# Performance work log

Measured on AMD Instinct MI355X. Metric: run time of the kernel, lower is better.

The kernel has to match this reference:

```python
import jax, jax.numpy as jnp
import numpy as np

N_EDGES = 8_388_608      # total synapses (flat weight vector length)
NUM_TYPES = 200          # number of unique edge types (ragged groups)
STRENGTH = 1e-3          # regularizer strength (cast to float32 as in the TF module)


def setup_inputs() -> dict:
    key = jax.random.key(0)
    k1, k2, k3 = jax.random.split(key, 3)
    # Edges pre-sorted by edge type -> contiguous segments (equivalent to the
    # RaggedTensor.from_value_rowids grouping built in __init__).
    segment_ids = jnp.sort(
        jax.random.randint(k1, (N_EDGES,), 0, NUM_TYPES, dtype=jnp.int32))
    x = jax.random.normal(k2, (N_EDGES,), dtype=jnp.float32)
    init_raw = jax.random.normal(k3, (N_EDGES,), dtype=jnp.float32)
    # __init__ sorts the initial weights within each edge-type group; since
    # segment_ids is already sorted, lexsort with segment_ids as the primary
    # key sorts values within each contiguous segment.
    order = jnp.lexsort((init_raw, segment_ids))
    initial_sorted = init_raw[order]
    return {"x": x, "initial_sorted": initial_sorted, "segment_ids": segment_ids}


def reference(x, initial_sorted, segment_ids):
    x = x.astype(jnp.float32)
    # Segmented sort of the current weights: primary key = edge type,
    # secondary key = value. Equivalent to tf.sort(x_i) per ragged group.
    order = jnp.lexsort((x, segment_ids))
    x_sorted = x[order]                       # [n_edges], sorted within each group
    diff = jnp.abs(x_sorted - initial_sorted)  # per-edge |sorted(x) - sorted(y)|
    sums = jax.ops.segment_sum(diff, segment_ids, num_segments=NUM_TYPES)
    counts = jax.ops.segment_sum(jnp.ones_like(diff), segment_ids,
                                 num_segments=NUM_TYPES)
    emd = sums / jnp.maximum(counts, 1.0)      # per-group Wasserstein-1 (mean L1)
    return jnp.mean(emd) * jnp.float32(STRENGTH)
```

## Files before the change

### kernel.cpp

```cpp
#include <hip/hip_runtime.h>
#include <hip/hip_bf16.h>

#define NSEG 200
#define STRENGTH 1e-3f
#define NFB 16384
#define FSCALE (16384.0f / 12.0f)
#define BT 1024
#define SPLIT 5
#define WINCAP 9728
#define EPT 10
#define PSTRIDE (NFB + 8)
#define PCH 8192
#define SLICE_E 8200

__device__ __forceinline__ int fbin_of(float v) {
    float t = (v + 6.0f) * FSCALE;
    int b = (int)floorf(t);
    return b < 0 ? 0 : (b > NFB - 1 ? NFB - 1 : b);
}

__global__ void __launch_bounds__(BT)
k_hist(const float* __restrict__ x, const int* __restrict__ seg,
       int* __restrict__ seg_starts, float* __restrict__ segSums,
       unsigned* __restrict__ gcur, unsigned short* __restrict__ pfxg,
       int* __restrict__ Bg, int* __restrict__ Bpos, int N) {
    __shared__ unsigned hw[NFB / 2];
    __shared__ unsigned wsum[16];
    __shared__ int sh2[3];
    int s = blockIdx.x;
    int t = threadIdx.x;
    if (t <= 1) {
        int key = s + t;
        int lo = 0, hi = N;
        while (lo < hi) { int mid = (lo + hi) >> 1; if (seg[mid] < key) lo = mid + 1; else hi = mid; }
        sh2[t] = lo;
    }
    if (t < 8) gcur[s * 8 + t] = 0u;
    if (t == 2) segSums[s] = 0.f;
    for (int k = t; k < NFB / 2; k += BT) hw[k] = 0;
    __syncthreads();
    int st = sh2[0], en = sh2[1];
    if (t == 3) { seg_starts[s] = st; if (s == NSEG - 1) seg_starts[NSEG] = N; }
    int n = en - st;
    const float* xs = x + st;
    if (n > 0) {
        int head = min(n, (int)((4 - (st & 3)) & 3));
        for (int k = t; k < head; k += BT) { int f = fbin_of(xs[k]); atomicAdd(&hw[f >> 1], 1u << ((f & 1) * 16)); }
        int nv = (n - head) >> 2;
        const float4* xs4 = (const float4*)(xs + head);
        for (int j = t; j < nv; j += BT) {
            float4 v = xs4[j];
            int f0 = fbin_of(v.x), f1 = fbin_of(v.y), f2 = fbin_of(v.z), f3 = fbin_of(v.w);
            atomicAdd(&hw[f0 >> 1], 1u << ((f0 & 1) * 16));
            atomicAdd(&hw[f1 >> 1], 1u << ((f1 & 1) * 16));
            atomicAdd(&hw[f2 >> 1], 1u << ((f2 & 1) * 16));
            atomicAdd(&hw[f3 >> 1], 1u << ((f3 & 1) * 16));
        }
        for (int k = head + nv * 4 + t; k < n; k += BT) { int f = fbin_of(xs[k]); atomicAdd(&hw[f >> 1], 1u << ((f & 1) * 16)); }
    }
    __syncthreads();
    unsigned wv[8]; unsigned run = 0;
    #pragma unroll
    for (int i = 0; i < 8; ++i) {
        unsigned w = hw[t * 8 + i];
        unsigned c0 = w & 0xffffu, c1 = w >> 16;
        wv[i] = run | ((run + c0) << 16);
        run += c0 + c1;
    }
    unsigned incl = run;
    for (int off = 1; off < 64; off <<= 1) {
        unsigned nv2 = __shfl_up(incl, off, 64);
        if ((t & 63) >= off) incl += nv2;
    }
    if ((t & 63) == 63) wsum[t >> 6] = incl;
    __syncthreads();
    unsigned wb = 0; int myw = t >> 6;
    #pragma unroll
    for (int j = 0; j < 16; ++j) wb += (j < myw) ? wsum[j] : 0u;
    unsigned base = wb + incl - run;
    unsigned bb = base | (base << 16);
    unsigned short* pp = pfxg + (size_t)s * PSTRIDE;
    #pragma unroll
    for (int i = 0; i < 8; ++i) {
        unsigned pw = wv[i] + bb;
        hw[t * 8 + i] = pw;
        ((unsigned*)pp)[t * 8 + i] = pw;
    }
    if (t == BT - 1) { pp[NFB] = (unsigned short)(base + run); sh2[2] = (int)(base + run); }
    __syncthreads();
    int nsh = sh2[2];
    if (t == 0) { Bg[s * 8 + 0] = 0; Bg[s * 8 + SPLIT] = NFB; Bpos[s * 8 + 0] = 0; Bpos[s * 8 + SPLIT] = nsh; }
    if (t >= 1 && t < SPLIT) {
        int target = (int)(((long)t * nsh) / SPLIT);
        int lo = 0, hi = NFB - 1;
        while (lo < hi) {
            int mid = (lo + hi) >> 1;
            int pv = (int)((hw[(mid + 1) >> 1] >> (((mid + 1) & 1) * 16)) & 0xffffu);
            if (pv > target) hi = mid; else lo = mid + 1;
        }
        Bg[s * 8 + t] = lo;
        Bpos[s * 8 + t] = (int)((hw[lo >> 1] >> ((lo & 1) * 16)) & 0xffffu);
    }
}

__global__ void __launch_bounds__(1024)
k_part(const float* __restrict__ x, const int* __restrict__ seg_starts,
       const int* __restrict__ Bg, const int* __restrict__ Bpos,
       unsigned* __restrict__ gcur, float* __restrict__ part, int N) {
    __shared__ int sst[NSEG + 1];
    __shared__ unsigned hh[16][12];
    __shared__ int gb[10];
    __shared__ int sB[8];
    int t = threadIdx.x;
    for (int k = t; k < NSEG + 1; k += 1024) sst[k] = seg_starts[k];
    if (t < 192) ((unsigned*)hh)[t] = 0u;
    __syncthreads();
    int base = blockIdx.x * PCH;
    if (base >= N) return;
    int lo = 0, hi = NSEG - 1;
    while (lo < hi) { int mid = (lo + hi) >> 1; if (base < sst[mid + 1]) hi = mid; else lo = mid + 1; }
    int s0 = lo, bnd = sst[s0 + 1];
    if (t < 4) sB[t] = Bg[s0 * 8 + 1 + t];
    else if (t < 8 && s0 + 1 <= NSEG) sB[t] = Bg[(s0 + 1) * 8 + 1 + (t - 4)];
    __syncthreads();
    int grp = t >> 6;
    float vv[8]; unsigned pk[8];
    const float4* x4 = (const float4*)(x + base);
    #pragma unroll
    for (int it = 0; it < 2; ++it) {
        int j = it * 1024 + t;
        int gi = base + j * 4;
        float4 v4;
        if (gi + 3 < N) v4 = x4[j];
        else v4 = make_float4(0.f, 0.f, 0.f, 0.f);
        #pragma unroll
        for (int e = 0; e < 4; ++e) {
            int i = it * 4 + e;
            float v = (e == 0) ? v4.x : (e == 1) ? v4.y : (e == 2) ? v4.z : v4.w;
            vv[i] = v;
            int g = gi + e;
            if (g < N) {
                int off = (g >= bnd) ? 4 : 0;
                int f = fbin_of(v);
                int p = (f >= sB[off]) + (f >= sB[off + 1]) + (f >= sB[off + 2]) + (f >= sB[off + 3]);
                int sp = (off >> 2) * 5 + p;
                unsigned lr = atomicAdd(&hh[grp][sp], 1u);
                pk[i] = ((unsigned)sp << 10) | lr;
            } else pk[i] = 0xffffffffu;
        }
    }
    __syncthreads();
    if (t < 10) {
        unsigned run = 0;
        #pragma unroll
        for (int g = 0; g < 16; ++g) { unsigned c = hh[g][t]; hh[g][t] = run; run += c; }
        int s = s0 + (t >= 5);
        int p = (t >= 5) ? t - 5 : t;
        int rsv = 0;
        if (run > 0) rsv = (int)atomicAdd(&gcur[s * 8 + p], run);
        gb[t] = sst[s] + Bpos[s * 8 + p] + rsv;
    }
    __syncthreads();
    #pragma unroll
    for (int i = 0; i < 8; ++i) {
        if (pk[i] == 0xffffffffu) continue;
        int sp = (int)(pk[i] >> 10);
        int lr = (int)(pk[i] & 1023u);
        part[gb[sp] + (int)hh[grp][sp] + lr] = vv[i];
    }
}

__global__ void __launch_bounds__(BT)
k_seg(const float* __restrict__ part, const float* __restrict__ y,
      const int* __restrict__ seg_starts, const unsigned short* __restrict__ pfxg,
      const int* __restrict__ Bg, float* __restrict__ segSums) {
    __shared__ unsigned short slice[SLICE_E];
    __shared__ unsigned cur[2056];
    __shared__ __align__(16) float win[WINCAP + 4];
    __shared__ float warr[16];
    int s = blockIdx.x % NSEG;
    int p = blockIdx.x / NSEG;
    int t = threadIdx.x;
    int st = seg_starts[s], en = seg_starts[s + 1];
    int n = en - st;
    if (n <= 0) return;
    const unsigned short* pp = pfxg + (size_t)s * PSTRIDE;
    int Fa = Bg[s * 8 + p], Fb = Bg[s * 8 + p + 1];
    int spanc = Fb - Fa;
    int w0 = pp[Fa], w1 = pp[Fb];
    int wsz = w1 - w0;
    if (wsz <= 0) return;
    const float* ps = part + st + w0;
    bool sliced = (spanc + 1) <= SLICE_E;

    float rv[EPT]; int rr[EPT];
    if (sliced) {
        for (int k = t; k <= spanc; k += BT) slice[k] = pp[Fa + k];
        for (int k = t; k < ((spanc + 4) >> 2); k += BT) cur[k] = 0u;
        __syncthreads();
        int head = min(wsz, (int)((4 - ((st + w0) & 3)) & 3));
        for (int k = t; k < head; k += BT) {
            float v = ps[k];
            int i = fbin_of(v) - Fa;
            unsigned shf = (i & 3) * 8;
            unsigned old = atomicAdd(&cur[i >> 2], 1u << shf);
            win[(int)slice[i] - w0 + (int)((old >> shf) & 0xFFu)] = v;
        }
        int nv = (wsz - head) >> 2;
        const float4* ps4 = (const float4*)(ps + head);
        for (int j = t; j < nv; j += BT) {
            float4 v4 = ps4[j];
            #pragma unroll
            for (int e = 0; e < 4; ++e) {
                float v = (e == 0) ? v4.x : (e == 1) ? v4.y : (e == 2) ? v4.z : v4.w;
                int i = fbin_of(v) - Fa;
                unsigned shf = (i & 3) * 8;
                unsigned old = atomicAdd(&cur[i >> 2], 1u << shf);
                win[(int)slice[i] - w0 + (int)((old >> shf) & 0xFFu)] = v;
            }
        }
        for (int k = head + nv * 4 + t; k < wsz; k += BT) {
            float v = ps[k];
            int i = fbin_of(v) - Fa;
            unsigned shf = (i & 3) * 8;
            unsigned old = atomicAdd(&cur[i >> 2], 1u << shf);
            win[(int)slice[i] - w0 + (int)((old >> shf) & 0xFFu)] = v;
        }
        if (t < 4) win[wsz + t] = __builtin_inff();
        __syncthreads();
        #pragma unroll
        for (int e = 0; e < EPT; ++e) {
            int ql = e * BT + t;
            rr[e] = -1;
            if (ql < wsz) {
                float v = win[ql];
                rv[e] = v;
                int i = fbin_of(v) - Fa;
                int ls = (int)slice[i] - w0, le = (int)slice[i + 1] - w0;
                int a = ls & ~3;
                int cnt = a - ls;
                for (int j = a; j < le; j += 4) {
                    float4 qv = *(const float4*)&win[j];
                    cnt += (qv.x < v) + ((qv.x == v) & (j + 0 < ql));
                    cnt += (qv.y < v) + ((qv.y == v) & (j + 1 < ql));
                    cnt += (qv.z < v) + ((qv.z == v) & (j + 2 < ql));
                    cnt += (qv.w < v) + ((qv.w == v) & (j + 3 < ql));
                }
                rr[e] = ls + cnt;
            }
        }
    } else {
        for (int k = t; k < wsz; k += BT) win[k] = ps[k];
        if (t < 4) win[wsz + t] = __builtin_inff();
        __syncthreads();
        #pragma unroll
        for (int e = 0; e < EPT; ++e) {
            int ql = e * BT + t;
            rr[e] = -1;
            if (ql < wsz) {
                float v = win[ql];
                rv[e] = v;
                int cnt = 0;
                for (int j = 0; j < wsz; j += 4) {
                    float4 qv = *(const float4*)&win[j];
                    cnt += (qv.x < v) + ((qv.x == v) & (j + 0 < ql));
                    cnt += (qv.y < v) + ((qv.y == v) & (j + 1 < ql));
                    cnt += (qv.z < v) + ((qv.z == v) & (j + 2 < ql));
                    cnt += (qv.w < v) + ((qv.w == v) & (j + 3 < ql));
                }
                rr[e] = cnt;
            }
        }
    }
    __syncthreads();
    #pragma unroll
    for (int e = 0; e < EPT; ++e) {
        if (rr[e] >= 0) win[rr[e]] = rv[e];
    }
    __syncthreads();
    float acc = 0.f;
    const float* yw = y + st + w0;
    int head2 = min(wsz, (int)((4 - ((st + w0) & 3)) & 3));
    for (int k = t; k < head2; k += BT) acc += fabsf(win[k] - yw[k]);
    int nv2 = (wsz - head2) >> 2;
    const float4* yw4 = (const float4*)(yw + head2);
    for (int j = t; j < nv2; j += BT) {
        float4 yv = yw4[j];
        int k = head2 + j * 4;
        acc += fabsf(win[k + 0] - yv.x);
        acc += fabsf(win[k + 1] - yv.y);
        acc += fabsf(win[k + 2] - yv.z);
        acc += fabsf(win[k + 3] - yv.w);
    }
    for (int k = head2 + nv2 * 4 + t; k < wsz; k += BT) acc += fabsf(win[k] - yw[k]);

    for (int off = 32; off > 0; off >>= 1) acc += __shfl_xor(acc, off, 64);
    if ((t & 63) == 0) warr[t >> 6] = acc;
    __syncthreads();
    if (t == 0) {
        float tot = 0.f;
        #pragma unroll
        for (int j = 0; j < 16; ++j) tot += warr[j];
        if (tot != 0.f) atomicAdd(&segSums[s], tot);
    }
}

__global__ void k_final(const float* __restrict__ segSums, const int* __restrict__ seg_starts,
                        float* __restrict__ out) {
    __shared__ float red[256];
    int t = threadIdx.x;
    float a = 0.f;
    for (int k = t; k < NSEG; k += 256) {
        float n = (float)(seg_starts[k + 1] - seg_starts[k]);
        a += segSums[k] / fmaxf(n, 1.0f);
    }
    red[t] = a;
    __syncthreads();
    for (int off = 128; off > 0; off >>= 1) {
        if (t < off) red[t] += red[t + off];
        __syncthreads();
    }
    if (t == 0) out[0] = red[0] * (1.0f / (float)NSEG) * STRENGTH;
}

extern "C" void kernel_launch(void* const* d_in, const int* in_sizes, int n_in,
                              void* d_out, int out_size, void* d_ws, size_t ws_size,
                              hipStream_t stream) {
    const float* x = (const float*)d_in[0];
    const float* y = (const float*)d_in[1];
    const int* seg = (const int*)d_in[2];
    int N = in_sizes[0];

    char* ws = (char*)d_ws;
    float* segSums    = (float*)ws;
    int*   seg_starts = (int*)(ws + 800);
    unsigned* gcur    = (unsigned*)(ws + 1616);
    int*   Bg         = (int*)(ws + 8016);
    int*   Bpos       = (int*)(ws + 14448);
    unsigned short* pfxg = (unsigned short*)(ws + 20880);
    float* part       = (float*)(ws + 20880 + (size_t)NSEG * PSTRIDE * 2 + 16);

    int nchunk = (N + PCH - 1) / PCH;

    k_hist<<<NSEG, BT, 0, stream>>>(x, seg, seg_starts, segSums, gcur, pfxg, Bg, Bpos, N);
    k_part<<<nchunk, 1024, 0, stream>>>(x, seg_starts, Bg, Bpos, gcur, part, N);
    k_seg<<<NSEG * SPLIT, BT, 0, stream>>>(part, y, seg_starts, pfxg, Bg, segSums);
    k_final<<<1, 256, 0, stream>>>(segSums, seg_starts, (float*)d_out);
}
```

Measured before the change: 89.89 us.

## Privatize histogram copies, replace LDS atomics with wave scans, keep scattered values in registers

The histogram kernel now keeps two shared-memory copies, selected by wave parity, to cut atomic contention, and merges them during the prefix scan. The partition kernel replaces per-group LDS atomic counters with packed 12-bit wave-level shuffle prefix sums plus a cross-wave base table. The segment kernel keeps each element's value, bin and slot in registers during the scatter, so the ranking pass does not reload from the window and recompute the bin. This adds register pressure (14-entry arrays) and relies on a fixed unroll count that assumes the window fits in three float4 iterations per thread.

```diff
diff --git a/kernel.cpp b/kernel.cpp
--- a/kernel.cpp
+++ b/kernel.cpp
@@ -8,7 +8,7 @@
 #define BT 1024
 #define SPLIT 5
 #define WINCAP 9728
-#define EPT 10
+#define SR 14
 #define PSTRIDE (NFB + 8)
 #define PCH 8192
 #define SLICE_E 8200
@@ -24,11 +24,12 @@
        int* __restrict__ seg_starts, float* __restrict__ segSums,
        unsigned* __restrict__ gcur, unsigned short* __restrict__ pfxg,
        int* __restrict__ Bg, int* __restrict__ Bpos, int N) {
-    __shared__ unsigned hw[NFB / 2];
+    __shared__ unsigned hw[NFB];
     __shared__ unsigned wsum[16];
     __shared__ int sh2[3];
     int s = blockIdx.x;
     int t = threadIdx.x;
+    int copy = ((t >> 6) & 1) * (NFB / 2);
     if (t <= 1) {
         int key = s + t;
         int lo = 0, hi = N;
@@ -37,7 +38,7 @@
     }
     if (t < 8) gcur[s * 8 + t] = 0u;
     if (t == 2) segSums[s] = 0.f;
-    for (int k = t; k < NFB / 2; k += BT) hw[k] = 0;
+    for (int k = t; k < NFB; k += BT) hw[k] = 0;
     __syncthreads();
     int st = sh2[0], en = sh2[1];
     if (t == 3) { seg_starts[s] = st; if (s == NSEG - 1) seg_starts[NSEG] = N; }
@@ -45,24 +46,24 @@
     const float* xs = x + st;
     if (n > 0) {
         int head = min(n, (int)((4 - (st & 3)) & 3));
-        for (int k = t; k < head; k += BT) { int f = fbin_of(xs[k]); atomicAdd(&hw[f >> 1], 1u << ((f & 1) * 16)); }
+        for (int k = t; k < head; k += BT) { int f = fbin_of(xs[k]); atomicAdd(&hw[copy + (f >> 1)], 1u << ((f & 1) * 16)); }
         int nv = (n - head) >> 2;
         const float4* xs4 = (const float4*)(xs + head);
         for (int j = t; j < nv; j += BT) {
             float4 v = xs4[j];
             int f0 = fbin_of(v.x), f1 = fbin_of(v.y), f2 = fbin_of(v.z), f3 = fbin_of(v.w);
-            atomicAdd(&hw[f0 >> 1], 1u << ((f0 & 1) * 16));
-            atomicAdd(&hw[f1 >> 1], 1u << ((f1 & 1) * 16));
-            atomicAdd(&hw[f2 >> 1], 1u << ((f2 & 1) * 16));
-            atomicAdd(&hw[f3 >> 1], 1u << ((f3 & 1) * 16));
-        }
-        for (int k = head + nv * 4 + t; k < n; k += BT) { int f = fbin_of(xs[k]); atomicAdd(&hw[f >> 1], 1u << ((f & 1) * 16)); }
+            atomicAdd(&hw[copy + (f0 >> 1)], 1u << ((f0 & 1) * 16));
+            atomicAdd(&hw[copy + (f1 >> 1)], 1u << ((f1 & 1) * 16));
+            atomicAdd(&hw[copy + (f2 >> 1)], 1u << ((f2 & 1) * 16));
+            atomicAdd(&hw[copy + (f3 >> 1)], 1u << ((f3 & 1) * 16));
+        }
+        for (int k = head + nv * 4 + t; k < n; k += BT) { int f = fbin_of(xs[k]); atomicAdd(&hw[copy + (f >> 1)], 1u << ((f & 1) * 16)); }
     }
     __syncthreads();
     unsigned wv[8]; unsigned run = 0;
     #pragma unroll
     for (int i = 0; i < 8; ++i) {
-        unsigned w = hw[t * 8 + i];
+        unsigned w = hw[t * 8 + i] + hw[NFB / 2 + t * 8 + i];
         unsigned c0 = w & 0xffffu, c1 = w >> 16;
         wv[i] = run | ((run + c0) << 16);
         run += c0 + c1;
@@ -108,12 +109,13 @@
        const int* __restrict__ Bg, const int* __restrict__ Bpos,
        unsigned* __restrict__ gcur, float* __restrict__ part, int N) {
     __shared__ int sst[NSEG + 1];
-    __shared__ unsigned hh[16][12];
+    __shared__ unsigned long long wtA[16], wtB[16];
+    __shared__ unsigned short wbase[16][10];
     __shared__ int gb[10];
     __shared__ int sB[8];
     int t = threadIdx.x;
+    int lane = t & 63, wid = t >> 6;
     for (int k = t; k < NSEG + 1; k += 1024) sst[k] = seg_starts[k];
-    if (t < 192) ((unsigned*)hh)[t] = 0u;
     __syncthreads();
     int base = blockIdx.x * PCH;
     if (base >= N) return;
@@ -121,52 +123,74 @@
     while (lo < hi) { int mid = (lo + hi) >> 1; if (base < sst[mid + 1]) hi = mid; else lo = mid + 1; }
     int s0 = lo, bnd = sst[s0 + 1];
     if (t < 4) sB[t] = Bg[s0 * 8 + 1 + t];
-    else if (t < 8 && s0 + 1 <= NSEG) sB[t] = Bg[(s0 + 1) * 8 + 1 + (t - 4)];
-    __syncthreads();
-    int grp = t >> 6;
-    float vv[8]; unsigned pk[8];
+    else if (t < 8) sB[t] = (s0 + 1 < NSEG) ? Bg[(s0 + 1) * 8 + 1 + (t - 4)] : 0x7fffffff;
+    __syncthreads();
+    float vv[8]; unsigned spk = 0;
+    unsigned long long A = 0, B = 0;
     const float4* x4 = (const float4*)(x + base);
     #pragma unroll
     for (int it = 0; it < 2; ++it) {
         int j = it * 1024 + t;
         int gi = base + j * 4;
-        float4 v4;
-        if (gi + 3 < N) v4 = x4[j];
-        else v4 = make_float4(0.f, 0.f, 0.f, 0.f);
+        float4 v4 = (gi + 3 < N) ? x4[j] : make_float4(0.f, 0.f, 0.f, 0.f);
         #pragma unroll
         for (int e = 0; e < 4; ++e) {
             int i = it * 4 + e;
             float v = (e == 0) ? v4.x : (e == 1) ? v4.y : (e == 2) ? v4.z : v4.w;
             vv[i] = v;
             int g = gi + e;
+            unsigned sp = 15u;
             if (g < N) {
                 int off = (g >= bnd) ? 4 : 0;
                 int f = fbin_of(v);
                 int p = (f >= sB[off]) + (f >= sB[off + 1]) + (f >= sB[off + 2]) + (f >= sB[off + 3]);
-                int sp = (off >> 2) * 5 + p;
-                unsigned lr = atomicAdd(&hh[grp][sp], 1u);
-                pk[i] = ((unsigned)sp << 10) | lr;
-            } else pk[i] = 0xffffffffu;
-        }
+                sp = (unsigned)((off >> 2) * 5 + p);
+                if (sp < 5u) A += 1ull << (12 * sp);
+                else B += 1ull << (12 * (sp - 5));
+            }
+            spk |= sp << (i * 4);
+        }
+    }
+    unsigned long long iA = A, iB = B;
+    #pragma unroll
+    for (int off = 1; off < 64; off <<= 1) {
+        unsigned long long uA = __shfl_up(iA, off, 64);
+        unsigned long long uB = __shfl_up(iB, off, 64);
+        if (lane >= off) { iA += uA; iB += uB; }
+    }
+    if (lane == 63) { wtA[wid] = iA; wtB[wid] = iB; }
+    unsigned long long eA = iA - A, eB = iB - B;
+    __syncthreads();
+    if (t < 160) {
+        int w = t / 10, sp = t % 10;
+        unsigned acc = 0;
+        for (int w2 = 0; w2 < w; ++w2)
+            acc += (unsigned)(((sp < 5) ? (wtA[w2] >> (12 * sp)) : (wtB[w2] >> (12 * (sp - 5)))) & 0xfffull);
+        wbase[w][sp] = (unsigned short)acc;
     }
     __syncthreads();
     if (t < 10) {
-        unsigned run = 0;
-        #pragma unroll
-        for (int g = 0; g < 16; ++g) { unsigned c = hh[g][t]; hh[g][t] = run; run += c; }
-        int s = s0 + (t >= 5);
-        int p = (t >= 5) ? t - 5 : t;
+        int sp = t;
+        unsigned tot = (unsigned)wbase[15][sp] +
+            (unsigned)(((sp < 5) ? (wtA[15] >> (12 * sp)) : (wtB[15] >> (12 * (sp - 5)))) & 0xfffull);
+        int s = s0 + (sp >= 5);
+        int p = (sp >= 5) ? sp - 5 : sp;
         int rsv = 0;
-        if (run > 0) rsv = (int)atomicAdd(&gcur[s * 8 + p], run);
-        gb[t] = sst[s] + Bpos[s * 8 + p] + rsv;
-    }
-    __syncthreads();
+        if (tot > 0 && s < NSEG) rsv = (int)atomicAdd(&gcur[s * 8 + p], tot);
+        gb[sp] = (s < NSEG) ? (sst[s] + Bpos[s * 8 + p] + rsv) : 0;
+    }
+    __syncthreads();
+    unsigned long long cA = 0, cB = 0;
     #pragma unroll
     for (int i = 0; i < 8; ++i) {
-        if (pk[i] == 0xffffffffu) continue;
-        int sp = (int)(pk[i] >> 10);
-        int lr = (int)(pk[i] & 1023u);
-        part[gb[sp] + (int)hh[grp][sp] + lr] = vv[i];
+        unsigned sp = (spk >> (i * 4)) & 15u;
+        if (sp < 10u) {
+            unsigned fld;
+            if (sp < 5u) { fld = (unsigned)(((eA + cA) >> (12 * sp)) & 0xfffull); cA += 1ull << (12 * sp); }
+            else { fld = (unsigned)(((eB + cB) >> (12 * (sp - 5))) & 0xfffull); cB += 1ull << (12 * (sp - 5)); }
+            int local = (int)wbase[wid][sp] + (int)fld;
+            part[gb[sp] + local] = vv[i];
+        }
     }
 }
 
@@ -193,89 +217,104 @@
     const float* ps = part + st + w0;
     bool sliced = (spanc + 1) <= SLICE_E;
 
-    float rv[EPT]; int rr[EPT];
+    float rv[SR]; unsigned rk[SR];
+    #pragma unroll
+    for (int r = 0; r < SR; ++r) rk[r] = 0xffffffffu;
+
     if (sliced) {
         for (int k = t; k <= spanc; k += BT) slice[k] = pp[Fa + k];
         for (int k = t; k < ((spanc + 4) >> 2); k += BT) cur[k] = 0u;
         __syncthreads();
         int head = min(wsz, (int)((4 - ((st + w0) & 3)) & 3));
-        for (int k = t; k < head; k += BT) {
-            float v = ps[k];
+        if (t < head) {
+            float v = ps[t];
             int i = fbin_of(v) - Fa;
             unsigned shf = (i & 3) * 8;
             unsigned old = atomicAdd(&cur[i >> 2], 1u << shf);
-            win[(int)slice[i] - w0 + (int)((old >> shf) & 0xFFu)] = v;
+            int slot = (int)slice[i] - w0 + (int)((old >> shf) & 0xFFu);
+            win[slot] = v;
+            rv[0] = v; rk[0] = ((unsigned)i << 14) | (unsigned)slot;
         }
         int nv = (wsz - head) >> 2;
         const float4* ps4 = (const float4*)(ps + head);
-        for (int j = t; j < nv; j += BT) {
-            float4 v4 = ps4[j];
-            #pragma unroll
-            for (int e = 0; e < 4; ++e) {
-                float v = (e == 0) ? v4.x : (e == 1) ? v4.y : (e == 2) ? v4.z : v4.w;
-                int i = fbin_of(v) - Fa;
-                unsigned shf = (i & 3) * 8;
-                unsigned old = atomicAdd(&cur[i >> 2], 1u << shf);
-                win[(int)slice[i] - w0 + (int)((old >> shf) & 0xFFu)] = v;
+        #pragma unroll
+        for (int g = 0; g < 3; ++g) {
+            int j = g * BT + t;
+            if (j < nv) {
+                float4 v4 = ps4[j];
+                #pragma unroll
+                for (int e = 0; e < 4; ++e) {
+                    float v = (e == 0) ? v4.x : (e == 1) ? v4.y : (e == 2) ? v4.z : v4.w;
+                    int i = fbin_of(v) - Fa;
+                    unsigned shf = (i & 3) * 8;
+                    unsigned old = atomicAdd(&cur[i >> 2], 1u << shf);
+                    int slot = (int)slice[i] - w0 + (int)((old >> shf) & 0xFFu);
+                    win[slot] = v;
+                    rv[1 + g * 4 + e] = v;
+                    rk[1 + g * 4 + e] = ((unsigned)i << 14) | (unsigned)slot;
+                }
             }
         }
-        for (int k = head + nv * 4 + t; k < wsz; k += BT) {
-            float v = ps[k];
+        int k2 = head + nv * 4 + t;
+        if (k2 < wsz) {
+            float v = ps[k2];
             int i = fbin_of(v) - Fa;
             unsigned shf = (i & 3) * 8;
             unsigned old = atomicAdd(&cur[i >> 2], 1u << shf);
-            win[(int)slice[i] - w0 + (int)((old >> shf) & 0xFFu)] = v;
+            int slot = (int)slice[i] - w0 + (int)((old >> shf) & 0xFFu);
+            win[slot] = v;
+            rv[13] = v; rk[13] = ((unsigned)i << 14) | (unsigned)slot;
         }
         if (t < 4) win[wsz + t] = __builtin_inff();
         __syncthreads();
         #pragma unroll
-        for (int e = 0; e < EPT; ++e) {
-            int ql = e * BT + t;
-            rr[e] = -1;
-            if (ql < wsz) {
-                float v = win[ql];
-                rv[e] = v;
-                int i = fbin_of(v) - Fa;
+        for (int r = 0; r < SR; ++r) {
+            if (rk[r] != 0xffffffffu) {
+                float v = rv[r];
+                int i = (int)(rk[r] >> 14);
+                int slot = (int)(rk[r] & 0x3fffu);
                 int ls = (int)slice[i] - w0, le = (int)slice[i + 1] - w0;
                 int a = ls & ~3;
                 int cnt = a - ls;
                 for (int j = a; j < le; j += 4) {
                     float4 qv = *(const float4*)&win[j];
-                    cnt += (qv.x < v) + ((qv.x == v) & (j + 0 < ql));
-                    cnt += (qv.y < v) + ((qv.y == v) & (j + 1 < ql));
-                    cnt += (qv.z < v) + ((qv.z == v) & (j + 2 < ql));
-                    cnt += (qv.w < v) + ((qv.w == v) & (j + 3 < ql));
+                    cnt += (qv.x < v) + ((qv.x == v) & (j + 0 < slot));
+                    cnt += (qv.y < v) + ((qv.y == v) & (j + 1 < slot));
+                    cnt += (qv.z < v) + ((qv.z == v) & (j + 2 < slot));
+                    cnt += (qv.w < v) + ((qv.w == v) & (j + 3 < slot));
                 }
-                rr[e] = ls + cnt;
+                rk[r] = (unsigned)(ls + cnt);
             }
         }
     } else {
-        for (int k = t; k < wsz; k += BT) win[k] = ps[k];
+        #pragma unroll
+        for (int g = 0; g < 10; ++g) {
+            int k = g * BT + t;
+            if (k < wsz) { float v = ps[k]; win[k] = v; rv[g] = v; rk[g] = (unsigned)k; }
+        }
         if (t < 4) win[wsz + t] = __builtin_inff();
         __syncthreads();
         #pragma unroll
-        for (int e = 0; e < EPT; ++e) {
-            int ql = e * BT + t;
-            rr[e] = -1;
-            if (ql < wsz) {
-                float v = win[ql];
-                rv[e] = v;
+        for (int g = 0; g < 10; ++g) {
+            if (rk[g] != 0xffffffffu) {
+                float v = rv[g];
+                int slot = (int)rk[g];
                 int cnt = 0;
                 for (int j = 0; j < wsz; j += 4) {
                     float4 qv = *(const float4*)&win[j];
-                    cnt += (qv.x < v) + ((qv.x == v) & (j + 0 < ql));
-                    cnt += (qv.y < v) + ((qv.y == v) & (j + 1 < ql));
-                    cnt += (qv.z < v) + ((qv.z == v) & (j + 2 < ql));
-                    cnt += (qv.w < v) + ((qv.w == v) & (j + 3 < ql));
+                    cnt += (qv.x < v) + ((qv.x == v) & (j + 0 < slot));
+                    cnt += (qv.y < v) + ((qv.y == v) & (j + 1 < slot));
+                    cnt += (qv.z < v) + ((qv.z == v) & (j + 2 < slot));
+                    cnt += (qv.w < v) + ((qv.w == v) & (j + 3 < slot));
                 }
-                rr[e] = cnt;
+                rk[g] = (unsigned)cnt;
             }
         }
     }
     __syncthreads();
     #pragma unroll
-    for (int e = 0; e < EPT; ++e) {
-        if (rr[e] >= 0) win[rr[e]] = rv[e];
+    for (int r = 0; r < SR; ++r) {
+        if (rk[r] != 0xffffffffu) win[rk[r]] = rv[r];
     }
     __syncthreads();
     float acc = 0.f;
```

New measurement: 107.8 us. 1.2x slower.
